# Optimization experiments

Hardware: AMD Instinct MI355X
Metric: run time of the kernel (lower is better)

## Reference

```python
import jax, jax.numpy as jnp
import numpy as np

V, E, H = 32000, 300, 1024
BS, S = 256, 512


def setup_inputs() -> dict:
    key = jax.random.key(0)
    ks = jax.random.split(key, 10)
    return {
        "current_indices": jax.random.randint(ks[0], (BS,), 0, V),
        "hiddens_from_prev_step": jax.random.normal(ks[1], (1, BS, H), jnp.float32),
        "encoder_outputs": jax.random.normal(ks[2], (BS, S, H), jnp.float32),
        "emb_table": jax.random.normal(ks[3], (V, E), jnp.float32) * 0.02,
        "W_ih": jax.random.normal(ks[4], (H, E + H), jnp.float32) * (1.0 / np.sqrt(E + H)),
        "b_ih": jnp.zeros((H,), jnp.float32),
        "W_hh": jax.random.normal(ks[5], (H, H), jnp.float32) * (1.0 / np.sqrt(H)),
        "b_hh": jnp.zeros((H,), jnp.float32),
        "fc_W": jax.random.normal(ks[6], (V, H), jnp.float32) * (1.0 / np.sqrt(H)),
        "fc_b": jnp.zeros((V,), jnp.float32),
    }


def reference(current_indices, hiddens_from_prev_step, encoder_outputs,
              emb_table, W_ih, b_ih, W_hh, b_hh, fc_W, fc_b):
    # eval mode: dropout is identity
    h = hiddens_from_prev_step[0]                      # (bs, H)
    emb = emb_table[current_indices]                   # (bs, E)
    # Bahdanau-dot attention: scores = enc @ h
    energy = jnp.einsum('bsh,bh->bs', encoder_outputs, h)      # (bs, S)
    attn = jax.nn.softmax(energy, axis=-1)                      # (bs, S)
    ctx = jnp.einsum('bsh,bs->bh', encoder_outputs, attn)       # (bs, H)
    x = jnp.concatenate([emb, ctx], axis=-1)                    # (bs, E+H)
    # single-step vanilla RNN (tanh)
    h_new = jnp.tanh(x @ W_ih.T + b_ih + h @ W_hh.T + b_hh)     # (bs, H)
    logits = h_new @ fc_W.T + fc_b                              # (bs, V)
    return logits, h_new[None], attn
```

## Files before the change

### kernel.cpp

```cpp
#include <hip/hip_runtime.h>
#include <hip/hip_bf16.h>
#include <math.h>

#define BS 256
#define SEQ 512
#define HID 1024
#define EMB 300
#define VOC 32000
#define XCAT 2368
#define XREAL 2348

typedef unsigned short u16;
typedef short bf16x8 __attribute__((ext_vector_type(8)));
typedef float f32x4 __attribute__((ext_vector_type(4)));

__device__ __forceinline__ u16 f2bf(float f) {
    union { float f; unsigned int u; } v; v.f = f;
    unsigned int u = v.u;
    unsigned int r = (u + 0x7FFFu + ((u >> 16) & 1u)) >> 16;
    return (u16)r;
}

__global__ __launch_bounds__(1024) void attn_kernel(
    const int* __restrict__ idx,
    const float* __restrict__ hiddens,
    const float* __restrict__ enc,
    const float* __restrict__ emb_table,
    float* __restrict__ attn_out,
    u16* __restrict__ xcat)
{
    __shared__ float ctx_sh[8][HID];
    __shared__ float ctx_red[HID];
    __shared__ float energy_sh[SEQ];
    __shared__ float mw_sh[16], lw_sh[16];

    const int b = blockIdx.x;
    const int tid = threadIdx.x;
    const int wave = tid >> 6, lane = tid & 63;
    const float* encb = enc + (size_t)b * SEQ * HID;
    const float* hb = hiddens + (size_t)b * HID;

    float4 hreg[4];
#pragma unroll
    for (int c = 0; c < 4; ++c)
        hreg[c] = *(const float4*)(hb + 4 * lane + 256 * c);

    float m = -INFINITY, l = 0.f;
    float4 ctx[4];
#pragma unroll
    for (int c = 0; c < 4; ++c) ctx[c] = make_float4(0.f, 0.f, 0.f, 0.f);

    float4 ev[4], nv[4];
    {
        const float* p0 = encb + (size_t)wave * HID + 4 * lane;
#pragma unroll
        for (int c = 0; c < 4; ++c) ev[c] = *(const float4*)(p0 + 256 * c);
    }

    for (int t = 0; t < 32; ++t) {
        const int s = wave + 16 * t;
        if (t < 31) {
            const float* pn = encb + (size_t)(s + 16) * HID + 4 * lane;
#pragma unroll
            for (int c = 0; c < 4; ++c) nv[c] = *(const float4*)(pn + 256 * c);
        }
        float part = 0.f;
#pragma unroll
        for (int c = 0; c < 4; ++c) {
            part += ev[c].x * hreg[c].x + ev[c].y * hreg[c].y
                  + ev[c].z * hreg[c].z + ev[c].w * hreg[c].w;
        }
#pragma unroll
        for (int off = 32; off > 0; off >>= 1)
            part += __shfl_xor(part, off);
        const float e = part;
        if (lane == 0) energy_sh[s] = e;

        const float mnew = fmaxf(m, e);
        const float scale = __expf(m - mnew);
        const float pp = __expf(e - mnew);
        l = l * scale + pp;
#pragma unroll
        for (int c = 0; c < 4; ++c) {
            ctx[c].x = ctx[c].x * scale + pp * ev[c].x;
            ctx[c].y = ctx[c].y * scale + pp * ev[c].y;
            ctx[c].z = ctx[c].z * scale + pp * ev[c].z;
            ctx[c].w = ctx[c].w * scale + pp * ev[c].w;
        }
        m = mnew;
#pragma unroll
        for (int c = 0; c < 4; ++c) ev[c] = nv[c];
    }

    if (lane == 0) { mw_sh[wave] = m; lw_sh[wave] = l; }
    __syncthreads();

    float mtot = -INFINITY;
#pragma unroll
    for (int w = 0; w < 16; ++w) mtot = fmaxf(mtot, mw_sh[w]);
    float ltot = 0.f;
#pragma unroll
    for (int w = 0; w < 16; ++w) ltot += lw_sh[w] * __expf(mw_sh[w] - mtot);
    const float cw = __expf(m - mtot);

    if (wave >= 8) {
#pragma unroll
        for (int c = 0; c < 4; ++c) {
            float4 v = make_float4(ctx[c].x * cw, ctx[c].y * cw,
                                   ctx[c].z * cw, ctx[c].w * cw);
            *(float4*)&ctx_sh[wave - 8][4 * lane + 256 * c] = v;
        }
    }
    __syncthreads();
    if (wave < 8) {
#pragma unroll
        for (int c = 0; c < 4; ++c) {
            float4* dst = (float4*)&ctx_sh[wave][4 * lane + 256 * c];
            float4 cur = *dst;
            cur.x += ctx[c].x * cw; cur.y += ctx[c].y * cw;
            cur.z += ctx[c].z * cw; cur.w += ctx[c].w * cw;
            *dst = cur;
        }
    }
    __syncthreads();

    {
        float ssum = 0.f;
#pragma unroll
        for (int w = 0; w < 8; ++w) ssum += ctx_sh[w][tid];
        ctx_red[tid] = ssum / ltot;
    }

    const float inv_l = 1.f / ltot;
    if (tid < SEQ)
        attn_out[(size_t)b * SEQ + tid] = __expf(energy_sh[tid] - mtot) * inv_l;
    __syncthreads();

    const int iidx = idx[b];
    const size_t row_off = (size_t)b * XCAT;
    for (int i = tid; i < XCAT; i += 1024) {
        float v;
        if (i < EMB)            v = emb_table[(size_t)iidx * EMB + i];
        else if (i < EMB + HID) v = ctx_red[i - EMB];
        else if (i < XREAL)     v = hb[i - (EMB + HID)];
        else                    v = 0.f;
        xcat[row_off + i] = f2bf(v);
    }
}

__global__ __launch_bounds__(256) void rnn_gemm(
    const u16* __restrict__ A,
    const float* __restrict__ W_ih,
    const float* __restrict__ W_hh,
    const float* __restrict__ b_ih,
    const float* __restrict__ b_hh,
    float* __restrict__ outh,
    u16* __restrict__ hbf)
{
    constexpr int LDSS = 72;
    __shared__ u16 Ash[256 * LDSS];
    __shared__ u16 Bsh[64 * LDSS];
    const int tid = threadIdx.x;
    const int wave = tid >> 6, lane = tid & 63;
    const int lane15 = lane & 15, quad = lane >> 4;
    const int nblk = blockIdx.x;
    const int arow = tid >> 3;
    const int k0 = (tid & 7) * 8;

    f32x4 acc[4][4];
#pragma unroll
    for (int i = 0; i < 4; ++i)
#pragma unroll
        for (int j = 0; j < 4; ++j) acc[i][j] = f32x4{0.f, 0.f, 0.f, 0.f};

    for (int kt = 0; kt < XCAT / 64; ++kt) {
#pragma unroll
        for (int p = 0; p < 8; ++p) {
            const int row = p * 32 + arow;
            uint4 v = *(const uint4*)(A + (size_t)row * XCAT + kt * 64 + k0);
            *(uint4*)&Ash[row * LDSS + k0] = v;
        }
#pragma unroll
        for (int p = 0; p < 2; ++p) {
            const int row = p * 32 + arow;
            const int j = nblk * 64 + row;
            const int kbase = kt * 64 + k0;
            alignas(16) u16 tmp[8];
#pragma unroll
            for (int e = 0; e < 8; ++e) {
                const int kg = kbase + e;
                float v;
                if (kg < EMB + HID)   v = W_ih[(size_t)j * (EMB + HID) + kg];
                else if (kg < XREAL)  v = W_hh[(size_t)j * HID + (kg - (EMB + HID))];
                else                  v = 0.f;
                tmp[e] = f2bf(v);
            }
            *(uint4*)&Bsh[row * LDSS + k0] = *(const uint4*)tmp;
        }
        __syncthreads();
#pragma unroll
        for (int ks = 0; ks < 64; ks += 32) {
            bf16x8 af[4], bfr[4];
#pragma unroll
            for (int mi = 0; mi < 4; ++mi)
                af[mi] = *(const bf16x8*)&Ash[(wave * 64 + mi * 16 + lane15) * LDSS + ks + quad * 8];
#pragma unroll
            for (int ni = 0; ni < 4; ++ni)
                bfr[ni] = *(const bf16x8*)&Bsh[(ni * 16 + lane15) * LDSS + ks + quad * 8];
#pragma unroll
            for (int mi = 0; mi < 4; ++mi)
#pragma unroll
                for (int ni = 0; ni < 4; ++ni)
                    acc[mi][ni] = __builtin_amdgcn_mfma_f32_16x16x32_bf16(
                        af[mi], bfr[ni], acc[mi][ni], 0, 0, 0);
        }
        __syncthreads();
    }

#pragma unroll
    for (int ni = 0; ni < 4; ++ni) {
        const int n = nblk * 64 + ni * 16 + lane15;
        const float bv = b_ih[n] + b_hh[n];
#pragma unroll
        for (int mi = 0; mi < 4; ++mi)
#pragma unroll
            for (int r = 0; r < 4; ++r) {
                const int mm = wave * 64 + mi * 16 + quad * 4 + r;
                const float hv = tanhf(acc[mi][ni][r] + bv);
                outh[(size_t)mm * HID + n] = hv;
                hbf[(size_t)mm * HID + n] = f2bf(hv);
            }
    }
}

__global__ __launch_bounds__(256) void fc_gemm(
    const u16* __restrict__ A,
    const float* __restrict__ W,
    const float* __restrict__ bias,
    float* __restrict__ out)
{
    constexpr int K = 1024, LDSS = 72;
    __shared__ u16 Ash[256 * LDSS];
    __shared__ u16 Bsh[64 * LDSS];
    const int tid = threadIdx.x;
    const int wave = tid >> 6, lane = tid & 63;
    const int lane15 = lane & 15, quad = lane >> 4;
    const int nblk = blockIdx.x;
    const int arow = tid >> 3;
    const int k0 = (tid & 7) * 8;

    f32x4 acc[4][4];
#pragma unroll
    for (int i = 0; i < 4; ++i)
#pragma unroll
        for (int j = 0; j < 4; ++j) acc[i][j] = f32x4{0.f, 0.f, 0.f, 0.f};

    for (int kt = 0; kt < K / 64; ++kt) {
#pragma unroll
        for (int p = 0; p < 8; ++p) {
            const int row = p * 32 + arow;
            uint4 v = *(const uint4*)(A + (size_t)row * K + kt * 64 + k0);
            *(uint4*)&Ash[row * LDSS + k0] = v;
        }
#pragma unroll
        for (int p = 0; p < 2; ++p) {
            const int row = p * 32 + arow;
            const float* src = W + (size_t)(nblk * 64 + row) * K + kt * 64 + k0;
            alignas(16) u16 tmp[8];
            float4 f0 = *(const float4*)(src);
            float4 f1 = *(const float4*)(src + 4);
            tmp[0] = f2bf(f0.x); tmp[1] = f2bf(f0.y);
            tmp[2] = f2bf(f0.z); tmp[3] = f2bf(f0.w);
            tmp[4] = f2bf(f1.x); tmp[5] = f2bf(f1.y);
            tmp[6] = f2bf(f1.z); tmp[7] = f2bf(f1.w);
            *(uint4*)&Bsh[row * LDSS + k0] = *(const uint4*)tmp;
        }
        __syncthreads();
#pragma unroll
        for (int ks = 0; ks < 64; ks += 32) {
            bf16x8 af[4], bfr[4];
#pragma unroll
            for (int mi = 0; mi < 4; ++mi)
                af[mi] = *(const bf16x8*)&Ash[(wave * 64 + mi * 16 + lane15) * LDSS + ks + quad * 8];
#pragma unroll
            for (int ni = 0; ni < 4; ++ni)
                bfr[ni] = *(const bf16x8*)&Bsh[(ni * 16 + lane15) * LDSS + ks + quad * 8];
#pragma unroll
            for (int mi = 0; mi < 4; ++mi)
#pragma unroll
                for (int ni = 0; ni < 4; ++ni)
                    acc[mi][ni] = __builtin_amdgcn_mfma_f32_16x16x32_bf16(
                        af[mi], bfr[ni], acc[mi][ni], 0, 0, 0);
        }
        __syncthreads();
    }

#pragma unroll
    for (int ni = 0; ni < 4; ++ni) {
        const int n = nblk * 64 + ni * 16 + lane15;
        const float bv = bias[n];
#pragma unroll
        for (int mi = 0; mi < 4; ++mi)
#pragma unroll
            for (int r = 0; r < 4; ++r) {
                const int mm = wave * 64 + mi * 16 + quad * 4 + r;
                out[(size_t)mm * VOC + n] = acc[mi][ni][r] + bv;
            }
    }
}

extern "C" void kernel_launch(void* const* d_in, const int* in_sizes, int n_in,
                              void* d_out, int out_size, void* d_ws, size_t ws_size,
                              hipStream_t stream) {
    (void)in_sizes; (void)n_in; (void)out_size; (void)ws_size;
    const int*   idx  = (const int*)d_in[0];
    const float* hid  = (const float*)d_in[1];
    const float* enc  = (const float*)d_in[2];
    const float* emb  = (const float*)d_in[3];
    const float* W_ih = (const float*)d_in[4];
    const float* b_ih = (const float*)d_in[5];
    const float* W_hh = (const float*)d_in[6];
    const float* b_hh = (const float*)d_in[7];
    const float* fc_W = (const float*)d_in[8];
    const float* fc_b = (const float*)d_in[9];

    float* out    = (float*)d_out;
    float* logits = out;
    float* hnew   = out + (size_t)BS * VOC;
    float* attn   = out + (size_t)BS * VOC + BS * HID;

    u16* xcat = (u16*)d_ws;
    u16* hbf  = (u16*)d_ws + (size_t)BS * XCAT;

    hipLaunchKernelGGL(attn_kernel, dim3(BS), dim3(1024), 0, stream,
                       idx, hid, enc, emb, attn, xcat);
    hipLaunchKernelGGL(rnn_gemm, dim3(HID / 64), dim3(256), 0, stream,
                       xcat, W_ih, W_hh, b_ih, b_hh, hnew, hbf);
    hipLaunchKernelGGL(fc_gemm, dim3(VOC / 64), dim3(256), 0, stream,
                       hbf, fc_W, fc_b, logits);
}
```

Measured before the change: 1.007 ms.

## Prepack RNN weights to bf16 and split RNN GEMM into per-wave 16x16 tiles

A new pre-pass kernel converts W_ih and W_hh into one padded bf16 matrix. The RNN GEMM is rewritten so each wave computes a single 16x16 output tile, reading A and the packed weights directly from global memory across 256 blocks instead of 16. The FC GEMM drops its shared-memory staging of A, loads A fragments straight from global memory, and uses nontemporal stores for the logits. The aim is to remove the under-parallelized RNN GEMM and its per-tile float-to-bf16 conversion, at the cost of an extra kernel launch, workspace traffic, and uncached global reads in place of LDS reuse.

```diff
diff --git a/kernel.cpp b/kernel.cpp
--- a/kernel.cpp
+++ b/kernel.cpp
@@ -9,6 +9,7 @@
 #define VOC 32000
 #define XCAT 2368
 #define XREAL 2348
+#define IH_K (EMB + HID)
 
 typedef unsigned short u16;
 typedef short bf16x8 __attribute__((ext_vector_type(8)));
@@ -19,6 +20,28 @@
     unsigned int u = v.u;
     unsigned int r = (u + 0x7FFFu + ((u >> 16) & 1u)) >> 16;
     return (u16)r;
+}
+
+__global__ __launch_bounds__(256) void pack_w(
+    const float* __restrict__ W_ih,
+    const float* __restrict__ W_hh,
+    u16* __restrict__ Wp)
+{
+    const int t = blockIdx.x * 256 + threadIdx.x;
+    const int base = t * 8;
+    const int n = base / XCAT;
+    const int k0 = base - n * XCAT;
+    alignas(16) u16 tmp[8];
+#pragma unroll
+    for (int e = 0; e < 8; ++e) {
+        const int kg = k0 + e;
+        float v;
+        if (kg < IH_K)       v = W_ih[(size_t)n * IH_K + kg];
+        else if (kg < XREAL) v = W_hh[(size_t)n * HID + (kg - IH_K)];
+        else                 v = 0.f;
+        tmp[e] = f2bf(v);
+    }
+    *(uint4*)(Wp + base) = *(const uint4*)tmp;
 }
 
 __global__ __launch_bounds__(1024) void attn_kernel(
@@ -148,17 +171,51 @@
     }
 }
 
-__global__ __launch_bounds__(256) void rnn_gemm(
+__global__ __launch_bounds__(256) void rnn_gemm2(
     const u16* __restrict__ A,
-    const float* __restrict__ W_ih,
-    const float* __restrict__ W_hh,
+    const u16* __restrict__ Wp,
     const float* __restrict__ b_ih,
     const float* __restrict__ b_hh,
     float* __restrict__ outh,
     u16* __restrict__ hbf)
 {
-    constexpr int LDSS = 72;
-    __shared__ u16 Ash[256 * LDSS];
+    const int tid = threadIdx.x;
+    const int wave = tid >> 6, lane = tid & 63;
+    const int lane15 = lane & 15, quad = lane >> 4;
+    const int gw = blockIdx.x * 4 + wave;
+    const int mt = gw >> 6;
+    const int nt = gw & 63;
+    const int m0 = mt * 16, n0 = nt * 16;
+
+    const u16* Ap = A  + (size_t)(m0 + lane15) * XCAT + quad * 8;
+    const u16* Bp = Wp + (size_t)(n0 + lane15) * XCAT + quad * 8;
+
+    f32x4 acc = f32x4{0.f, 0.f, 0.f, 0.f};
+#pragma unroll 2
+    for (int k = 0; k < XCAT; k += 32) {
+        bf16x8 a  = *(const bf16x8*)(Ap + k);
+        bf16x8 bv = *(const bf16x8*)(Bp + k);
+        acc = __builtin_amdgcn_mfma_f32_16x16x32_bf16(a, bv, acc, 0, 0, 0);
+    }
+
+    const int n = n0 + lane15;
+    const float bv = b_ih[n] + b_hh[n];
+#pragma unroll
+    for (int r = 0; r < 4; ++r) {
+        const int mm = m0 + quad * 4 + r;
+        const float hv = tanhf(acc[r] + bv);
+        outh[(size_t)mm * HID + n] = hv;
+        hbf[(size_t)mm * HID + n] = f2bf(hv);
+    }
+}
+
+__global__ __launch_bounds__(256) void fc_gemm2(
+    const u16* __restrict__ A,
+    const float* __restrict__ W,
+    const float* __restrict__ bias,
+    float* __restrict__ out)
+{
+    constexpr int K = 1024, LDSS = 72;
     __shared__ u16 Bsh[64 * LDSS];
     const int tid = threadIdx.x;
     const int wave = tid >> 6, lane = tid & 63;
@@ -173,95 +230,9 @@
 #pragma unroll
         for (int j = 0; j < 4; ++j) acc[i][j] = f32x4{0.f, 0.f, 0.f, 0.f};
 
-    for (int kt = 0; kt < XCAT / 64; ++kt) {
-#pragma unroll
-        for (int p = 0; p < 8; ++p) {
-            const int row = p * 32 + arow;
-            uint4 v = *(const uint4*)(A + (size_t)row * XCAT + kt * 64 + k0);
-            *(uint4*)&Ash[row * LDSS + k0] = v;
-        }
-#pragma unroll
-        for (int p = 0; p < 2; ++p) {
-            const int row = p * 32 + arow;
-            const int j = nblk * 64 + row;
-            const int kbase = kt * 64 + k0;
-            alignas(16) u16 tmp[8];
-#pragma unroll
-            for (int e = 0; e < 8; ++e) {
-                const int kg = kbase + e;
-                float v;
-                if (kg < EMB + HID)   v = W_ih[(size_t)j * (EMB + HID) + kg];
-                else if (kg < XREAL)  v = W_hh[(size_t)j * HID + (kg - (EMB + HID))];
-                else                  v = 0.f;
-                tmp[e] = f2bf(v);
-            }
-            *(uint4*)&Bsh[row * LDSS + k0] = *(const uint4*)tmp;
-        }
-        __syncthreads();
-#pragma unroll
-        for (int ks = 0; ks < 64; ks += 32) {
-            bf16x8 af[4], bfr[4];
-#pragma unroll
-            for (int mi = 0; mi < 4; ++mi)
-                af[mi] = *(const bf16x8*)&Ash[(wave * 64 + mi * 16 + lane15) * LDSS + ks + quad * 8];
-#pragma unroll
-            for (int ni = 0; ni < 4; ++ni)
-                bfr[ni] = *(const bf16x8*)&Bsh[(ni * 16 + lane15) * LDSS + ks + quad * 8];
-#pragma unroll
-            for (int mi = 0; mi < 4; ++mi)
-#pragma unroll
-                for (int ni = 0; ni < 4; ++ni)
-                    acc[mi][ni] = __builtin_amdgcn_mfma_f32_16x16x32_bf16(
-                        af[mi], bfr[ni], acc[mi][ni], 0, 0, 0);
-        }
-        __syncthreads();
-    }
-
-#pragma unroll
-    for (int ni = 0; ni < 4; ++ni) {
-        const int n = nblk * 64 + ni * 16 + lane15;
-        const float bv = b_ih[n] + b_hh[n];
-#pragma unroll
-        for (int mi = 0; mi < 4; ++mi)
-#pragma unroll
-            for (int r = 0; r < 4; ++r) {
-                const int mm = wave * 64 + mi * 16 + quad * 4 + r;
-                const float hv = tanhf(acc[mi][ni][r] + bv);
-                outh[(size_t)mm * HID + n] = hv;
-                hbf[(size_t)mm * HID + n] = f2bf(hv);
-            }
-    }
-}
-
-__global__ __launch_bounds__(256) void fc_gemm(
-    const u16* __restrict__ A,
-    const float* __restrict__ W,
-    const float* __restrict__ bias,
-    float* __restrict__ out)
-{
-    constexpr int K = 1024, LDSS = 72;
-    __shared__ u16 Ash[256 * LDSS];
-    __shared__ u16 Bsh[64 * LDSS];
-    const int tid = threadIdx.x;
-    const int wave = tid >> 6, lane = tid & 63;
-    const int lane15 = lane & 15, quad = lane >> 4;
-    const int nblk = blockIdx.x;
-    const int arow = tid >> 3;
-    const int k0 = (tid & 7) * 8;
-
-    f32x4 acc[4][4];
-#pragma unroll
-    for (int i = 0; i < 4; ++i)
-#pragma unroll
-        for (int j = 0; j < 4; ++j) acc[i][j] = f32x4{0.f, 0.f, 0.f, 0.f};
+    const u16* Abase = A + (size_t)(wave * 64 + lane15) * K + quad * 8;
 
     for (int kt = 0; kt < K / 64; ++kt) {
-#pragma unroll
-        for (int p = 0; p < 8; ++p) {
-            const int row = p * 32 + arow;
-            uint4 v = *(const uint4*)(A + (size_t)row * K + kt * 64 + k0);
-            *(uint4*)&Ash[row * LDSS + k0] = v;
-        }
 #pragma unroll
         for (int p = 0; p < 2; ++p) {
             const int row = p * 32 + arow;
@@ -281,7 +252,7 @@
             bf16x8 af[4], bfr[4];
 #pragma unroll
             for (int mi = 0; mi < 4; ++mi)
-                af[mi] = *(const bf16x8*)&Ash[(wave * 64 + mi * 16 + lane15) * LDSS + ks + quad * 8];
+                af[mi] = *(const bf16x8*)(Abase + (size_t)mi * 16 * K + kt * 64 + ks);
 #pragma unroll
             for (int ni = 0; ni < 4; ++ni)
                 bfr[ni] = *(const bf16x8*)&Bsh[(ni * 16 + lane15) * LDSS + ks + quad * 8];
@@ -304,7 +275,8 @@
 #pragma unroll
             for (int r = 0; r < 4; ++r) {
                 const int mm = wave * 64 + mi * 16 + quad * 4 + r;
-                out[(size_t)mm * VOC + n] = acc[mi][ni][r] + bv;
+                __builtin_nontemporal_store(acc[mi][ni][r] + bv,
+                                            &out[(size_t)mm * VOC + n]);
             }
     }
 }
@@ -330,12 +302,15 @@
     float* attn   = out + (size_t)BS * VOC + BS * HID;
 
     u16* xcat = (u16*)d_ws;
-    u16* hbf  = (u16*)d_ws + (size_t)BS * XCAT;
-
+    u16* hbf  = xcat + (size_t)BS * XCAT;
+    u16* Wp   = hbf + (size_t)BS * HID;
+
+    hipLaunchKernelGGL(pack_w, dim3((HID * XCAT) / (256 * 8)), dim3(256), 0, stream,
+                       W_ih, W_hh, Wp);
     hipLaunchKernelGGL(attn_kernel, dim3(BS), dim3(1024), 0, stream,
                        idx, hid, enc, emb, attn, xcat);
-    hipLaunchKernelGGL(rnn_gemm, dim3(HID / 64), dim3(256), 0, stream,
-                       xcat, W_ih, W_hh, b_ih, b_hh, hnew, hbf);
-    hipLaunchKernelGGL(fc_gemm, dim3(VOC / 64), dim3(256), 0, stream,
+    hipLaunchKernelGGL(rnn_gemm2, dim3(BS), dim3(256), 0, stream,
+                       xcat, Wp, b_ih, b_hh, hnew, hbf);
+    hipLaunchKernelGGL(fc_gemm2, dim3(VOC / 64), dim3(256), 0, stream,
                        hbf, fc_W, fc_b, logits);
 }
```

Result: faster. 851.8 us (-15.4%).
